# Kernel optimization log

Measured on AMD Instinct MI355X. Metric: run time of the kernel, lower is better.

The kernel has to match this reference:

```python
import jax, jax.numpy as jnp
import numpy as np

N, IN_F, H, D = 4096, 256, 4, 64  # nodes, in_features, num_heads, head_dim
NEG_BIG = -9e15


def setup_inputs() -> dict:
    key = jax.random.key(0)
    k1, k2, k3, k4, k5 = jax.random.split(key, 5)
    x = jax.random.normal(k1, (N, IN_F), dtype=jnp.float32)
    adj = jax.random.randint(k2, (N, N), 0, 2, dtype=jnp.int32)
    # xavier-uniform-scale init for W: [in_features, H*D]
    lim_w = float(np.sqrt(6.0 / (IN_F + H * D)))
    W = jax.random.uniform(k3, (IN_F, H * D), minval=-lim_w, maxval=lim_w, dtype=jnp.float32)
    # a: [2*D, 1] split into a1 (dest half) and a2 (source half)
    lim_a = float(np.sqrt(6.0 / (2 * D + 1)))
    a1 = jax.random.uniform(k4, (D,), minval=-lim_a, maxval=lim_a, dtype=jnp.float32)
    a2 = jax.random.uniform(k5, (D,), minval=-lim_a, maxval=lim_a, dtype=jnp.float32)
    return {"x": x, "adj": adj, "W": W, "a1": a1, "a2": a2}


def reference(x, adj, W, a1, a2):
    n = x.shape[0]
    h = (x @ W).reshape(n, H, D)                      # [N, H, D]
    # e[i,j,h] = leaky_relu(<h_i, a1> + <h_j, a2>)  (== concat([h_i,h_j]) @ a)
    si = jnp.einsum("nhd,d->nh", h, a1)               # [N, H]
    sj = jnp.einsum("nhd,d->nh", h, a2)               # [N, H]
    e = jax.nn.leaky_relu(si[:, None, :] + sj[None, :, :], negative_slope=0.2)
    e = jnp.where(adj[:, :, None] > 0, e, NEG_BIG)    # mask non-edges
    att = jax.nn.softmax(e, axis=1)                   # softmax over neighbors j
    out = jnp.einsum("ijh,jhd->ihd", att, h)          # per-head aggregation
    return out.reshape(n, H * D)                      # concat heads
```

## Files before the change

kernel.cpp:

```cpp
#include <hip/hip_runtime.h>
#include <hip/hip_bf16.h>


typedef __bf16 bf16x8 __attribute__((ext_vector_type(8)));
typedef float floatx4 __attribute__((ext_vector_type(4)));

#define LOG2E 1.4426950408889634f
#define NN 4096

__device__ __forceinline__ void gl16(const void* g, void* l) {
  __builtin_amdgcn_global_load_lds(
      (const __attribute__((address_space(1))) unsigned int*)g,
      (__attribute__((address_space(3))) unsigned int*)l, 16, 0, 0);
}

__global__ __launch_bounds__(256) void gat_prep(
    const float* __restrict__ x, const float* __restrict__ W,
    const float* __restrict__ a1, const float* __restrict__ a2,
    const int* __restrict__ adj, __bf16* __restrict__ hTf,
    float* __restrict__ siT, float2* __restrict__ vv2T, float* __restrict__ sjm,
    unsigned char* __restrict__ adjb) {
  const int b = blockIdx.x;
  const int t = threadIdx.x;

  if (b >= 512) {
    int T = (b - 512) * 256 + t;
    const int stride = 2048 * 256;
#pragma unroll
    for (int it = 0; it < 4; ++it, T += stride) {
      const int* p = adj + (size_t)T * 8;
      int4 a = *(const int4*)p;
      int4 bb = *(const int4*)(p + 4);
      unsigned int m = 0;
      m |= (a.x != 0) ? 1u : 0u;
      m |= (a.y != 0) ? 2u : 0u;
      m |= (a.z != 0) ? 4u : 0u;
      m |= (a.w != 0) ? 8u : 0u;
      m |= (bb.x != 0) ? 16u : 0u;
      m |= (bb.y != 0) ? 32u : 0u;
      m |= (bb.z != 0) ? 64u : 0u;
      m |= (bb.w != 0) ? 128u : 0u;
      adjb[T] = (unsigned char)m;
    }
    return;
  }

  __shared__ float hl[32 * 68];
  __shared__ float sjb[32];
  const int it = b & 127, hh = b >> 7;
  const int i0 = it * 32, c0 = hh * 64;
  const int tr = t >> 4, tc = t & 15;

  float acc[2][4] = {{0.f,0.f,0.f,0.f},{0.f,0.f,0.f,0.f}};
  const float* xr = x + (size_t)(i0 + tr * 2) * 256;
  const float* wp = W + c0 + tc * 4;
  for (int k = 0; k < 256; k += 4) {
    float4 xv0 = *(const float4*)(xr + k);
    float4 xv1 = *(const float4*)(xr + 256 + k);
    float xs[2][4] = {{xv0.x, xv0.y, xv0.z, xv0.w},
                      {xv1.x, xv1.y, xv1.z, xv1.w}};
#pragma unroll
    for (int kk = 0; kk < 4; ++kk) {
      float4 wv = *(const float4*)(wp + (size_t)(k + kk) * 256);
#pragma unroll
      for (int i = 0; i < 2; ++i) {
        acc[i][0] = fmaf(xs[i][kk], wv.x, acc[i][0]);
        acc[i][1] = fmaf(xs[i][kk], wv.y, acc[i][1]);
        acc[i][2] = fmaf(xs[i][kk], wv.z, acc[i][2]);
        acc[i][3] = fmaf(xs[i][kk], wv.w, acc[i][3]);
      }
    }
  }

  float4 a1v = *(const float4*)(a1 + tc * 4);
  float4 a2v = *(const float4*)(a2 + tc * 4);
#pragma unroll
  for (int i = 0; i < 2; ++i) {
    float s1 = acc[i][0]*a1v.x + acc[i][1]*a1v.y + acc[i][2]*a1v.z + acc[i][3]*a1v.w;
    float s2 = acc[i][0]*a2v.x + acc[i][1]*a2v.y + acc[i][2]*a2v.z + acc[i][3]*a2v.w;
#pragma unroll
    for (int off = 1; off < 16; off <<= 1) {
      s1 += __shfl_xor(s1, off);
      s2 += __shfl_xor(s2, off);
    }
    if (tc == 0) {
      int r = tr * 2 + i;
      siT[hh * NN + i0 + r] = s1 * LOG2E;
      float sjs = s2 * LOG2E;
      vv2T[hh * NN + i0 + r] =
          make_float2(__builtin_amdgcn_exp2f(sjs), __builtin_amdgcn_exp2f(0.2f * sjs));
      sjb[r] = sjs;
    }
    *(float4*)&hl[(tr * 2 + i) * 68 + tc * 4] =
        make_float4(acc[i][0], acc[i][1], acc[i][2], acc[i][3]);
  }
  __syncthreads();

  if (t < 32) {
    float v = sjb[t];
#pragma unroll
    for (int off = 1; off < 32; off <<= 1) v = fmaxf(v, __shfl_xor(v, off));
    if (t == 0) sjm[it * 4 + hh] = v;
  }

  const int nt = t >> 6, lane = t & 63, quad = lane >> 4, l16 = lane & 15;
  bf16x8 h0;
#pragma unroll
  for (int jj = 0; jj < 8; ++jj)
    h0[jj] = (__bf16)hl[(quad * 8 + jj) * 68 + nt * 16 + l16];
  *(bf16x8*)((char*)hTf + ((((size_t)hh * 128 + it) * 4 + nt) << 10) + (lane << 4)) = h0;
}

__global__ __launch_bounds__(256, 2) void gat_attn(
    const __bf16* __restrict__ hTf, const float* __restrict__ siT,
    const float2* __restrict__ vv2T, const float* __restrict__ sjm,
    const unsigned int* __restrict__ adjw,
    float* __restrict__ pacc, float* __restrict__ pl) {
  __shared__ __align__(16) char lds[65536];
  const int t = threadIdx.x;
  const int w = t >> 6, lane = t & 63, quad = lane >> 4, l16 = lane & 15;
  const int i0 = blockIdx.x * 64, hh = blockIdx.y, s = blockIdx.z;
  const int jbeg = s * 2048;

  const char* hsrc = (const char*)hTf +
      (((size_t)hh * 128 + (jbeg >> 5) + w * 2) << 12) + (lane << 4);
  const float2* vw = vv2T + (size_t)hh * NN + jbeg + w * 64;

  const unsigned int* mp[4];
#pragma unroll
  for (int mt = 0; mt < 4; ++mt)
    mp[mt] = adjw + (size_t)(i0 + mt * 16 + l16) * 128 + (jbeg >> 5) + w * 2;

  uint2 mc[4], mn[4];
  float4 qc[2][4], qn[2][4];
#pragma unroll
  for (int mt = 0; mt < 4; ++mt) mc[mt] = *(const uint2*)mp[mt];
#pragma unroll
  for (int k = 0; k < 2; ++k) {
    const float4* qp = (const float4*)(vw + k * 32 + quad * 8);
#pragma unroll
    for (int c = 0; c < 4; ++c) qc[k][c] = qp[c];
  }
#pragma unroll
  for (int k = 0; k < 2; ++k)
#pragma unroll
    for (int nt = 0; nt < 4; ++nt)
      gl16(hsrc + ((k * 4 + nt) << 10),
           lds + (((w * 8 + k * 4 + nt) << 10) + (lane << 4)));

  float vv = fmaxf(sjm[lane * 4 + hh], sjm[(lane + 64) * 4 + hh]);
#pragma unroll
  for (int off = 1; off < 64; off <<= 1) vv = fmaxf(vv, __shfl_xor(vv, off));
  float u[4], u2[4];
#pragma unroll
  for (int mt = 0; mt < 4; ++mt) {
    float sis = siT[hh * NN + i0 + mt * 16 + l16];
    float tt = sis + vv;
    float m = fmaxf(tt, 0.2f * tt);
    u[mt] = __builtin_amdgcn_exp2f(sis - m);
    u2[mt] = __builtin_amdgcn_exp2f(0.2f * sis - m);
  }

  bf16x8 ones;
#pragma unroll
  for (int ii = 0; ii < 8; ++ii) ones[ii] = (__bf16)1.0f;

  floatx4 zv = {0.f, 0.f, 0.f, 0.f};
  floatx4 acc[4][4], lacc[4];
#pragma unroll
  for (int mt = 0; mt < 4; ++mt) {
    lacc[mt] = zv;
#pragma unroll
    for (int nt = 0; nt < 4; ++nt) acc[mt][nt] = zv;
  }

  __syncthreads();

  for (int win = 0; win < 8; ++win) {
    const int p = win & 1;
    const char* hb = lds + p * 32768;

    if (win + 1 < 8) {
#pragma unroll
      for (int mt = 0; mt < 4; ++mt)
        mn[mt] = *(const uint2*)(mp[mt] + (win + 1) * 8);
#pragma unroll
      for (int k = 0; k < 2; ++k) {
        const float4* qp = (const float4*)(vw + (win + 1) * 256 + k * 32 + quad * 8);
#pragma unroll
        for (int c = 0; c < 4; ++c) qn[k][c] = qp[c];
      }
      char* hbn = lds + (p ^ 1) * 32768;
      const char* hs = hsrc + (win + 1) * 32768;
#pragma unroll
      for (int k = 0; k < 2; ++k)
#pragma unroll
        for (int nt = 0; nt < 4; ++nt)
          gl16(hs + ((k * 4 + nt) << 10),
               hbn + (((w * 8 + k * 4 + nt) << 10) + (lane << 4)));
    }

#pragma unroll
    for (int k = 0; k < 2; ++k) {
      bf16x8 bfr[4];
#pragma unroll
      for (int nt = 0; nt < 4; ++nt)
        bfr[nt] = *(const bf16x8*)(hb + ((w * 8 + k * 4 + nt) << 10) + (lane << 4));
#pragma unroll
      for (int mt = 0; mt < 4; ++mt) {
        unsigned int m8 = (k ? mc[mt].y : mc[mt].x) >> (quad * 8);
        bf16x8 af;
#pragma unroll
        for (int c = 0; c < 4; ++c) {
          float p0 = fmaxf(u[mt] * qc[k][c].x, u2[mt] * qc[k][c].y);
          float p1 = fmaxf(u[mt] * qc[k][c].z, u2[mt] * qc[k][c].w);
          int b0 = ((int)(m8 << (31 - 2 * c))) >> 31;
          int b1 = ((int)(m8 << (30 - 2 * c))) >> 31;
          af[2 * c]     = (__bf16)__uint_as_float(__float_as_uint(p0) & (unsigned)b0);
          af[2 * c + 1] = (__bf16)__uint_as_float(__float_as_uint(p1) & (unsigned)b1);
        }
#pragma unroll
        for (int nt = 0; nt < 4; ++nt)
          acc[mt][nt] = __builtin_amdgcn_mfma_f32_16x16x32_bf16(af, bfr[nt],
                                                                acc[mt][nt], 0, 0, 0);
        lacc[mt] = __builtin_amdgcn_mfma_f32_16x16x32_bf16(af, ones, lacc[mt], 0, 0, 0);
      }
    }
#pragma unroll
    for (int mt = 0; mt < 4; ++mt) mc[mt] = mn[mt];
#pragma unroll
    for (int k = 0; k < 2; ++k)
#pragma unroll
      for (int c = 0; c < 4; ++c) qc[k][c] = qn[k][c];
    __syncthreads();
  }

  float* accs = (float*)lds;
  float* lsum = (float*)(lds + 34816);
  if (w < 2) {
#pragma unroll
    for (int mt = 0; mt < 4; ++mt)
#pragma unroll
      for (int reg = 0; reg < 4; ++reg) {
        int row = mt * 16 + quad * 4 + reg;
        float* ap = accs + (w * 64 + row) * 68;
#pragma unroll
        for (int nt = 0; nt < 4; ++nt)
          ap[nt * 16 + l16] = acc[mt][nt][reg];
        if (l16 == 0) lsum[w * 64 + row] = lacc[mt][reg];
      }
  }
  __syncthreads();
  if (w >= 2) {
    const int bb = w - 2;
#pragma unroll
    for (int mt = 0; mt < 4; ++mt)
#pragma unroll
      for (int reg = 0; reg < 4; ++reg) {
        int row = mt * 16 + quad * 4 + reg;
        float* ap = accs + (bb * 64 + row) * 68;
#pragma unroll
        for (int nt = 0; nt < 4; ++nt)
          ap[nt * 16 + l16] += acc[mt][nt][reg];
        if (l16 == 0) lsum[bb * 64 + row] += lacc[mt][reg];
      }
  }
  __syncthreads();

  const int r = t >> 2, cb = (t & 3) * 16;
  float* op = pacc + (size_t)s * NN * 256 + (size_t)(i0 + r) * 256 + hh * 64 + cb;
#pragma unroll
  for (int c4 = 0; c4 < 4; ++c4) {
    int c = cb + c4 * 4;
    float4 o;
    o.x = accs[r * 68 + c + 0] + accs[(64 + r) * 68 + c + 0];
    o.y = accs[r * 68 + c + 1] + accs[(64 + r) * 68 + c + 1];
    o.z = accs[r * 68 + c + 2] + accs[(64 + r) * 68 + c + 2];
    o.w = accs[r * 68 + c + 3] + accs[(64 + r) * 68 + c + 3];
    *(float4*)(op + c4 * 4) = o;
  }
  if (t < 64)
    pl[(size_t)s * NN * 4 + (i0 + t) * 4 + hh] = lsum[t] + lsum[64 + t];
}

__global__ __launch_bounds__(256) void gat_reduce(
    const float* __restrict__ pacc, const float* __restrict__ pl,
    float* __restrict__ out) {
  const int e4 = blockIdx.x * 256 + threadIdx.x;
  const int e = e4 * 4;
  const int i = e >> 8;
  const int h = (e & 255) >> 6;
  float4 a0 = *(const float4*)(pacc + e);
  float4 a1 = *(const float4*)(pacc + (size_t)NN * 256 + e);
  float l = pl[i * 4 + h] + pl[(size_t)NN * 4 + i * 4 + h];
  float inv = 1.0f / l;
  *(float4*)(out + e) = make_float4((a0.x + a1.x) * inv, (a0.y + a1.y) * inv,
                                    (a0.z + a1.z) * inv, (a0.w + a1.w) * inv);
}

extern "C" void kernel_launch(void* const* d_in, const int* in_sizes, int n_in,
                              void* d_out, int out_size, void* d_ws, size_t ws_size,
                              hipStream_t stream) {
  const float* x  = (const float*)d_in[0];
  const int*   adj = (const int*)d_in[1];
  const float* W  = (const float*)d_in[2];
  const float* a1 = (const float*)d_in[3];
  const float* a2 = (const float*)d_in[4];
  float* out = (float*)d_out;
  char* ws = (char*)d_ws;

  __bf16* hTf  = (__bf16*)ws;
  float*  siT  = (float*)(ws + 2097152);
  float2* vv2T = (float2*)(ws + 2162688);
  float*  sjm  = (float*)(ws + 2293760);
  unsigned char* adjb = (unsigned char*)(ws + 2295808);
  float*  pacc = (float*)(ws + 4392960);
  float*  pl   = (float*)(ws + 12781568);

  gat_prep<<<2560, 256, 0, stream>>>(x, W, a1, a2, adj, hTf, siT, vv2T, sjm, adjb);
  gat_attn<<<dim3(64, 4, 2), 256, 0, stream>>>(hTf, siT, vv2T, sjm,
                                               (const unsigned int*)adjb, pacc, pl);
  gat_reduce<<<1024, 256, 0, stream>>>(pacc, pl, out);
}
```

Baseline: 157.2 us.

## Split adjacency packing into LDS-staged kernel and shrink projection tiles

Moves the adjacency-to-bitmask packing out of the fused prep kernel into its own kernel that stages 16K ints per block into LDS with global_load_lds and emits 16-bit masks per thread. The projection kernel now uses 16-row tiles (1024 blocks, launch bounds raised to 4 waves/SIMD) with a single row per thread. The attention kernel's sjm max reads four entries to match the finer tiling. This aims to stream the 64 MB adjacency read more efficiently and raise occupancy of the GEMM, at the cost of an extra kernel launch and less register reuse of W.

```diff
diff --git a/kernel.cpp b/kernel.cpp
--- a/kernel.cpp
+++ b/kernel.cpp
@@ -14,101 +14,108 @@
       (__attribute__((address_space(3))) unsigned int*)l, 16, 0, 0);
 }
 
-__global__ __launch_bounds__(256) void gat_prep(
+__global__ __launch_bounds__(256) void gat_pack(const int* __restrict__ adj,
+                                                unsigned short* __restrict__ adjm) {
+  __shared__ __align__(16) int buf[4096];
+  const int t = threadIdx.x, w = t >> 6, lane = t & 63;
+  const int b = blockIdx.x;
+  const int* src = adj + (size_t)b * 16384;
+
+  for (int s = 0; s < 4; ++s) {
+    const int* sp = src + s * 4096 + w * 1024 + lane * 4;
+    int* dp = buf + w * 1024 + lane * 4;
+#pragma unroll
+    for (int r = 0; r < 4; ++r)
+      gl16(sp + r * 256, dp + r * 256);
+    __syncthreads();
+    const int4* rp = (const int4*)(buf + t * 16);
+    int4 v0 = rp[0], v1 = rp[1], v2 = rp[2], v3 = rp[3];
+    int vs[16] = {v0.x, v0.y, v0.z, v0.w, v1.x, v1.y, v1.z, v1.w,
+                  v2.x, v2.y, v2.z, v2.w, v3.x, v3.y, v3.z, v3.w};
+    unsigned int m = 0;
+#pragma unroll
+    for (int q = 0; q < 16; ++q) m |= (vs[q] != 0) ? (1u << q) : 0u;
+    adjm[(size_t)(b * 4 + s) * 256 + t] = (unsigned short)m;
+    __syncthreads();
+  }
+}
+
+__global__ __launch_bounds__(256, 4) void gat_prep(
     const float* __restrict__ x, const float* __restrict__ W,
     const float* __restrict__ a1, const float* __restrict__ a2,
-    const int* __restrict__ adj, __bf16* __restrict__ hTf,
-    float* __restrict__ siT, float2* __restrict__ vv2T, float* __restrict__ sjm,
-    unsigned char* __restrict__ adjb) {
-  const int b = blockIdx.x;
-  const int t = threadIdx.x;
-
-  if (b >= 512) {
-    int T = (b - 512) * 256 + t;
-    const int stride = 2048 * 256;
-#pragma unroll
-    for (int it = 0; it < 4; ++it, T += stride) {
-      const int* p = adj + (size_t)T * 8;
-      int4 a = *(const int4*)p;
-      int4 bb = *(const int4*)(p + 4);
-      unsigned int m = 0;
-      m |= (a.x != 0) ? 1u : 0u;
-      m |= (a.y != 0) ? 2u : 0u;
-      m |= (a.z != 0) ? 4u : 0u;
-      m |= (a.w != 0) ? 8u : 0u;
-      m |= (bb.x != 0) ? 16u : 0u;
-      m |= (bb.y != 0) ? 32u : 0u;
-      m |= (bb.z != 0) ? 64u : 0u;
-      m |= (bb.w != 0) ? 128u : 0u;
-      adjb[T] = (unsigned char)m;
-    }
-    return;
-  }
-
-  __shared__ float hl[32 * 68];
-  __shared__ float sjb[32];
-  const int it = b & 127, hh = b >> 7;
-  const int i0 = it * 32, c0 = hh * 64;
+    __bf16* __restrict__ hTf, float* __restrict__ siT, float2* __restrict__ vv2T,
+    float* __restrict__ sjm) {
+  __shared__ float hl[16 * 68];
+  __shared__ float sjb[16];
+  const int b = blockIdx.x, t = threadIdx.x;
+  const int it = b & 255, hh = b >> 8;
+  const int i0 = it * 16, c0 = hh * 64;
   const int tr = t >> 4, tc = t & 15;
 
-  float acc[2][4] = {{0.f,0.f,0.f,0.f},{0.f,0.f,0.f,0.f}};
-  const float* xr = x + (size_t)(i0 + tr * 2) * 256;
+  float acc[4] = {0.f, 0.f, 0.f, 0.f};
+  const float* xr = x + (size_t)(i0 + tr) * 256;
   const float* wp = W + c0 + tc * 4;
+#pragma unroll 4
   for (int k = 0; k < 256; k += 4) {
-    float4 xv0 = *(const float4*)(xr + k);
-    float4 xv1 = *(const float4*)(xr + 256 + k);
-    float xs[2][4] = {{xv0.x, xv0.y, xv0.z, xv0.w},
-                      {xv1.x, xv1.y, xv1.z, xv1.w}};
-#pragma unroll
-    for (int kk = 0; kk < 4; ++kk) {
-      float4 wv = *(const float4*)(wp + (size_t)(k + kk) * 256);
-#pragma unroll
-      for (int i = 0; i < 2; ++i) {
-        acc[i][0] = fmaf(xs[i][kk], wv.x, acc[i][0]);
-        acc[i][1] = fmaf(xs[i][kk], wv.y, acc[i][1]);
-        acc[i][2] = fmaf(xs[i][kk], wv.z, acc[i][2]);
-        acc[i][3] = fmaf(xs[i][kk], wv.w, acc[i][3]);
-      }
-    }
+    float4 xv = *(const float4*)(xr + k);
+    float4 wv0 = *(const float4*)(wp + (size_t)k * 256);
+    float4 wv1 = *(const float4*)(wp + (size_t)(k + 1) * 256);
+    float4 wv2 = *(const float4*)(wp + (size_t)(k + 2) * 256);
+    float4 wv3 = *(const float4*)(wp + (size_t)(k + 3) * 256);
+    acc[0] = fmaf(xv.x, wv0.x, acc[0]);
+    acc[1] = fmaf(xv.x, wv0.y, acc[1]);
+    acc[2] = fmaf(xv.x, wv0.z, acc[2]);
+    acc[3] = fmaf(xv.x, wv0.w, acc[3]);
+    acc[0] = fmaf(xv.y, wv1.x, acc[0]);
+    acc[1] = fmaf(xv.y, wv1.y, acc[1]);
+    acc[2] = fmaf(xv.y, wv1.z, acc[2]);
+    acc[3] = fmaf(xv.y, wv1.w, acc[3]);
+    acc[0] = fmaf(xv.z, wv2.x, acc[0]);
+    acc[1] = fmaf(xv.z, wv2.y, acc[1]);
+    acc[2] = fmaf(xv.z, wv2.z, acc[2]);
+    acc[3] = fmaf(xv.z, wv2.w, acc[3]);
+    acc[0] = fmaf(xv.w, wv3.x, acc[0]);
+    acc[1] = fmaf(xv.w, wv3.y, acc[1]);
+    acc[2] = fmaf(xv.w, wv3.z, acc[2]);
+    acc[3] = fmaf(xv.w, wv3.w, acc[3]);
   }
 
   float4 a1v = *(const float4*)(a1 + tc * 4);
   float4 a2v = *(const float4*)(a2 + tc * 4);
-#pragma unroll
-  for (int i = 0; i < 2; ++i) {
-    float s1 = acc[i][0]*a1v.x + acc[i][1]*a1v.y + acc[i][2]*a1v.z + acc[i][3]*a1v.w;
-    float s2 = acc[i][0]*a2v.x + acc[i][1]*a2v.y + acc[i][2]*a2v.z + acc[i][3]*a2v.w;
-#pragma unroll
-    for (int off = 1; off < 16; off <<= 1) {
-      s1 += __shfl_xor(s1, off);
-      s2 += __shfl_xor(s2, off);
-    }
-    if (tc == 0) {
-      int r = tr * 2 + i;
-      siT[hh * NN + i0 + r] = s1 * LOG2E;
-      float sjs = s2 * LOG2E;
-      vv2T[hh * NN + i0 + r] =
-          make_float2(__builtin_amdgcn_exp2f(sjs), __builtin_amdgcn_exp2f(0.2f * sjs));
-      sjb[r] = sjs;
-    }
-    *(float4*)&hl[(tr * 2 + i) * 68 + tc * 4] =
-        make_float4(acc[i][0], acc[i][1], acc[i][2], acc[i][3]);
-  }
+  float s1 = acc[0]*a1v.x + acc[1]*a1v.y + acc[2]*a1v.z + acc[3]*a1v.w;
+  float s2 = acc[0]*a2v.x + acc[1]*a2v.y + acc[2]*a2v.z + acc[3]*a2v.w;
+#pragma unroll
+  for (int off = 1; off < 16; off <<= 1) {
+    s1 += __shfl_xor(s1, off);
+    s2 += __shfl_xor(s2, off);
+  }
+  if (tc == 0) {
+    siT[hh * NN + i0 + tr] = s1 * LOG2E;
+    float sjs = s2 * LOG2E;
+    vv2T[hh * NN + i0 + tr] =
+        make_float2(__builtin_amdgcn_exp2f(sjs), __builtin_amdgcn_exp2f(0.2f * sjs));
+    sjb[tr] = sjs;
+  }
+  *(float4*)&hl[tr * 68 + tc * 4] = make_float4(acc[0], acc[1], acc[2], acc[3]);
   __syncthreads();
 
-  if (t < 32) {
+  if (t < 16) {
     float v = sjb[t];
 #pragma unroll
-    for (int off = 1; off < 32; off <<= 1) v = fmaxf(v, __shfl_xor(v, off));
+    for (int off = 1; off < 16; off <<= 1) v = fmaxf(v, __shfl_xor(v, off));
     if (t == 0) sjm[it * 4 + hh] = v;
   }
 
   const int nt = t >> 6, lane = t & 63, quad = lane >> 4, l16 = lane & 15;
-  bf16x8 h0;
-#pragma unroll
-  for (int jj = 0; jj < 8; ++jj)
-    h0[jj] = (__bf16)hl[(quad * 8 + jj) * 68 + nt * 16 + l16];
-  *(bf16x8*)((char*)hTf + ((((size_t)hh * 128 + it) * 4 + nt) << 10) + (lane << 4)) = h0;
+  const int c = it >> 1, half = it & 1;
+  if ((quad >> 1) == half) {
+    const int lr0 = (quad & 1) * 8;
+    bf16x8 h0;
+#pragma unroll
+    for (int jj = 0; jj < 8; ++jj)
+      h0[jj] = (__bf16)hl[(lr0 + jj) * 68 + nt * 16 + l16];
+    *(bf16x8*)((char*)hTf + ((((size_t)hh * 128 + c) * 4 + nt) << 10) + (lane << 4)) = h0;
+  }
 }
 
 __global__ __launch_bounds__(256, 2) void gat_attn(
@@ -148,7 +155,8 @@
       gl16(hsrc + ((k * 4 + nt) << 10),
            lds + (((w * 8 + k * 4 + nt) << 10) + (lane << 4)));
 
-  float vv = fmaxf(sjm[lane * 4 + hh], sjm[(lane + 64) * 4 + hh]);
+  float vv = fmaxf(fmaxf(sjm[lane * 4 + hh], sjm[(lane + 64) * 4 + hh]),
+                   fmaxf(sjm[(lane + 128) * 4 + hh], sjm[(lane + 192) * 4 + hh]));
 #pragma unroll
   for (int off = 1; off < 64; off <<= 1) vv = fmaxf(vv, __shfl_xor(vv, off));
   float u[4], u2[4];
@@ -313,11 +321,12 @@
   float*  siT  = (float*)(ws + 2097152);
   float2* vv2T = (float2*)(ws + 2162688);
   float*  sjm  = (float*)(ws + 2293760);
-  unsigned char* adjb = (unsigned char*)(ws + 2295808);
-  float*  pacc = (float*)(ws + 4392960);
-  float*  pl   = (float*)(ws + 12781568);
-
-  gat_prep<<<2560, 256, 0, stream>>>(x, W, a1, a2, adj, hTf, siT, vv2T, sjm, adjb);
+  unsigned char* adjb = (unsigned char*)(ws + 2297856);
+  float*  pacc = (float*)(ws + 4395008);
+  float*  pl   = (float*)(ws + 12783616);
+
+  gat_pack<<<1024, 256, 0, stream>>>(adj, (unsigned short*)adjb);
+  gat_prep<<<1024, 256, 0, stream>>>(x, W, a1, a2, hTf, siT, vv2T, sjm);
   gat_attn<<<dim3(64, 4, 2), 256, 0, stream>>>(hTf, siT, vv2T, sjm,
                                                (const unsigned int*)adjb, pacc, pl);
   gat_reduce<<<1024, 256, 0, stream>>>(pacc, pl, out);
```

After: 175.9 us. 11.9% more time.
